# Kernel optimization log

Measured on AMD Instinct MI355X. Metric: run time of the kernel, lower is better.

## Reference

```python
import jax, jax.numpy as jnp
import numpy as np

H = 16          # num_heads
EPS = 1e-6      # RMSNorm eps


def setup_inputs() -> dict:
    key = jax.random.key(0)
    ks = jax.random.split(key, 5)
    B, N, D = 4, 4096, 1024
    x = jax.random.normal(ks[0], (B, N, D), dtype=jnp.float32)
    q = jax.random.normal(ks[1], (D,), dtype=jnp.float32)
    k = jax.random.normal(ks[2], (D,), dtype=jnp.float32)
    log_decay = jax.random.normal(ks[3], (H,), dtype=jnp.float32)
    norm_weight = jnp.ones((D,), dtype=jnp.float32)
    o_w = jax.random.normal(ks[4], (D, D), dtype=jnp.float32) * 0.02
    return {"x": x, "q": q, "k": k, "log_decay": log_decay,
            "norm_weight": norm_weight, "o_w": o_w}


def reference(x, q, k, log_decay, norm_weight, o_w):
    b, n, dm = x.shape
    dh = dm // H
    qh = q.reshape(H, dh)            # per-head query vector (constant over b, n)
    kh = k.reshape(H, dh)            # per-head key vector
    v = x.reshape(b, n, H, dh)       # values = input tokens
    # exp(logsigmoid(a)) == sigmoid(a): per-head decay in (0, 1)
    lam = jax.nn.sigmoid(log_decay)  # (H,)

    def step(S, v_t):
        # S: (b, H, dh, dh) recurrent state;  v_t: (b, H, dh)
        S = lam[None, :, None, None] * S + kh[None, :, :, None] * v_t[:, :, None, :]
        o_t = jnp.einsum('hd,bhdv->bhv', qh, S)
        return S, o_t

    S0 = jnp.zeros((b, H, dh, dh), dtype=x.dtype)
    _, o = jax.lax.scan(step, S0, jnp.moveaxis(v, 1, 0))  # o: (n, b, H, dh)
    o = jnp.moveaxis(o, 0, 1).reshape(b, n, dm)

    # RMSNorm over the channel dim
    o = o * jax.lax.rsqrt(jnp.mean(o * o, axis=-1, keepdims=True) + EPS) * norm_weight
    # o_proj (no bias)
    return o @ o_w.T
```

## Files before the change

### kernel.cpp

```cpp
#include <hip/hip_runtime.h>
#include <hip/hip_bf16.h>
#include <cstdint>
#include <cstddef>

#define HH   16
#define BB   4
#define NN   4096
#define DD   1024
#define MM   (BB * NN)
#define NC   128
#define LC   32
#define EPSV 1e-6f

typedef short short8 __attribute__((ext_vector_type(8)));
typedef float floatx4 __attribute__((ext_vector_type(4)));

__device__ __forceinline__ void async_copy16(const void* g, void* l) {
    __builtin_amdgcn_global_load_lds(
        (const __attribute__((address_space(1))) void*)g,
        (__attribute__((address_space(3))) void*)l, 16, 0, 0);
}

__device__ __forceinline__ uint2 pack_bf16x4(float a, float b, float c, float d) {
    union { __hip_bfloat16 h[4]; uint2 u; } cv;
    cv.h[0] = __float2bfloat16(a); cv.h[1] = __float2bfloat16(b);
    cv.h[2] = __float2bfloat16(c); cv.h[3] = __float2bfloat16(d);
    return cv.u;
}

__global__ void k_meta(const float* __restrict__ q, const float* __restrict__ k,
                       const float* __restrict__ ld, float* __restrict__ meta) {
    int tid = threadIdx.x;
    float p = q[tid] * k[tid];
    #pragma unroll
    for (int off = 32; off > 0; off >>= 1) p += __shfl_xor(p, off);
    if ((tid & 63) == 0) meta[16 + (tid >> 6)] = p;
    if (tid < HH) meta[tid] = 1.f / (1.f + expf(-ld[tid]));
}

__global__ void k_wconv(const float* __restrict__ ow, const float* __restrict__ nw,
                        __hip_bfloat16* __restrict__ wp) {
    size_t i4 = (size_t)blockIdx.x * 256 + threadIdx.x;
    int j = (int)((i4 * 4) & (DD - 1));
    float4 v = ((const float4*)ow)[i4];
    ((uint2*)wp)[i4] = pack_bf16x4(v.x * nw[j], v.y * nw[j + 1],
                                   v.z * nw[j + 2], v.w * nw[j + 3]);
}

__global__ void k_chunk_end(const float* __restrict__ x, const float* __restrict__ meta,
                            float* __restrict__ E) {
    int b = blockIdx.x >> 7, c = blockIdx.x & (NC - 1);
    int j4 = threadIdx.x;
    float lam = meta[(j4 * 4) >> 6];
    const float4* xp = (const float4*)(x + ((size_t)(b * NN + c * LC)) * DD) + j4;
    float4 e = {0.f, 0.f, 0.f, 0.f};
    #pragma unroll
    for (int t = 0; t < LC; ++t) {
        float4 v = xp[(size_t)t * (DD / 4)];
        e.x = fmaf(lam, e.x, v.x); e.y = fmaf(lam, e.y, v.y);
        e.z = fmaf(lam, e.z, v.z); e.w = fmaf(lam, e.w, v.w);
    }
    ((float4*)(E + (size_t)blockIdx.x * DD))[j4] = e;
}

__global__ void k_carry(const float* __restrict__ meta, const float* __restrict__ E,
                        float* __restrict__ P) {
    __shared__ float tile[NC][33];
    int b = blockIdx.x >> 5, jg = blockIdx.x & 31;
    int tid = threadIdx.x;
    int cc = tid >> 5, jj = tid & 31;
    #pragma unroll
    for (int it = 0; it < 16; ++it) {
        int c = it * 8 + cc;
        tile[c][jj] = E[(size_t)(b * NC + c) * DD + jg * 32 + jj];
    }
    __syncthreads();
    if (tid < 32) {
        int j = jg * 32 + tid;
        float lam = meta[j >> 6];
        float lamL = lam;
        lamL *= lamL; lamL *= lamL; lamL *= lamL; lamL *= lamL; lamL *= lamL;
        float p = 0.f;
        for (int c = 0; c < NC; ++c) {
            float e = tile[c][tid];
            tile[c][tid] = p;
            p = fmaf(lamL, p, e);
        }
    }
    __syncthreads();
    #pragma unroll
    for (int it = 0; it < 16; ++it) {
        int c = it * 8 + cc;
        P[(size_t)(b * NC + c) * DD + jg * 32 + jj] = tile[c][jj];
    }
}

__global__ void k_scan(const float* __restrict__ x, const float* __restrict__ meta,
                       const float* __restrict__ P, __hip_bfloat16* __restrict__ obf,
                       float* __restrict__ sumsq) {
    int b = blockIdx.x >> 7, c = blockIdx.x & (NC - 1);
    int j4 = threadIdx.x;
    int h = (j4 * 4) >> 6;
    float lam = meta[h];
    float ch  = meta[16 + h];
    int row0 = b * NN + c * LC;
    const float4* xp = (const float4*)(x + (size_t)row0 * DD) + j4;
    float4 y = ((const float4*)(P + (size_t)blockIdx.x * DD))[j4];
    int lane0 = ((threadIdx.x & 63) == 0);
    for (int t = 0; t < LC; ++t) {
        float4 v = xp[(size_t)t * (DD / 4)];
        y.x = fmaf(lam, y.x, v.x); y.y = fmaf(lam, y.y, v.y);
        y.z = fmaf(lam, y.z, v.z); y.w = fmaf(lam, y.w, v.w);
        float ox = ch * y.x, oy = ch * y.y, oz = ch * y.z, ow = ch * y.w;
        ((uint2*)(obf + (size_t)(row0 + t) * DD))[j4] = pack_bf16x4(ox, oy, oz, ow);
        float s = ox * ox + oy * oy + oz * oz + ow * ow;
        #pragma unroll
        for (int off = 32; off > 0; off >>= 1) s += __shfl_xor(s, off);
        if (lane0) atomicAdd(&sumsq[row0 + t], s);
    }
}

__launch_bounds__(256)
__global__ void k_gemm(const __hip_bfloat16* __restrict__ A,
                       const __hip_bfloat16* __restrict__ W,
                       const float* __restrict__ sumsq, float* __restrict__ out) {
    __shared__ __attribute__((aligned(16))) short sA[128 * 64];
    __shared__ __attribute__((aligned(16))) short sB[128 * 64];
    const int tid = threadIdx.x;
    const int l = tid & 63, w = tid >> 6;
    const int wm = w >> 1, wn = w & 1;
    const int g = blockIdx.x;
    const int bm = g & 127, bn = g >> 7;
    const int m0 = bm * 128, n0 = bn * 128;
    const short* Ag = (const short*)A;
    const short* Wg = (const short*)W;

    floatx4 acc[4][4] = {};

    int srow[4], scol[4];
    #pragma unroll
    for (int i = 0; i < 4; ++i) {
        int s = i * 256 + tid;
        srow[i] = s >> 3;
        scol[i] = ((s & 7) ^ ((s >> 3) & 7)) * 8;
    }

    for (int kt = 0; kt < 16; ++kt) {
        const int k0 = kt * 64;
        #pragma unroll
        for (int i = 0; i < 4; ++i) {
            async_copy16(Ag + (size_t)(m0 + srow[i]) * 1024 + k0 + scol[i],
                         (char*)sA + i * 4096 + w * 1024);
            async_copy16(Wg + (size_t)(n0 + srow[i]) * 1024 + k0 + scol[i],
                         (char*)sB + i * 4096 + w * 1024);
        }
        __syncthreads();
        #pragma unroll
        for (int ks = 0; ks < 2; ++ks) {
            short8 af[4], bf[4];
            #pragma unroll
            for (int mt = 0; mt < 4; ++mt) {
                int row = wm * 64 + mt * 16 + (l & 15);
                int c8  = (ks * 4 + (l >> 4)) ^ (row & 7);
                af[mt] = *(const short8*)(sA + row * 64 + c8 * 8);
            }
            #pragma unroll
            for (int nt = 0; nt < 4; ++nt) {
                int row = wn * 64 + nt * 16 + (l & 15);
                int c8  = (ks * 4 + (l >> 4)) ^ (row & 7);
                bf[nt] = *(const short8*)(sB + row * 64 + c8 * 8);
            }
            #pragma unroll
            for (int mt = 0; mt < 4; ++mt)
                #pragma unroll
                for (int nt = 0; nt < 4; ++nt)
                    acc[mt][nt] = __builtin_amdgcn_mfma_f32_16x16x32_bf16(af[mt], bf[nt], acc[mt][nt], 0, 0, 0);
        }
        __syncthreads();
    }

    #pragma unroll
    for (int mt = 0; mt < 4; ++mt) {
        #pragma unroll
        for (int r = 0; r < 4; ++r) {
            int mrow = m0 + wm * 64 + mt * 16 + (l >> 4) * 4 + r;
            float rs = rsqrtf(sumsq[mrow] * (1.f / 1024.f) + EPSV);
            #pragma unroll
            for (int nt = 0; nt < 4; ++nt) {
                int col = n0 + wn * 64 + nt * 16 + (l & 15);
                out[(size_t)mrow * 1024 + col] = acc[mt][nt][r] * rs;
            }
        }
    }
}

extern "C" void kernel_launch(void* const* d_in, const int* in_sizes, int n_in,
                              void* d_out, int out_size, void* d_ws, size_t ws_size,
                              hipStream_t stream) {
    const float* x  = (const float*)d_in[0];
    const float* q  = (const float*)d_in[1];
    const float* k  = (const float*)d_in[2];
    const float* ld = (const float*)d_in[3];
    const float* nw = (const float*)d_in[4];
    const float* ow = (const float*)d_in[5];
    float* out = (float*)d_out;

    char* ws = (char*)d_ws;
    float* meta  = (float*)(ws + 0);
    float* sumsq = (float*)(ws + 256);
    float* E     = (float*)(ws + 65792);
    float* P     = (float*)(ws + 2162944);
    __hip_bfloat16* Wp  = (__hip_bfloat16*)(ws + 4260096);
    __hip_bfloat16* Obf = (__hip_bfloat16*)(ws + 6357248);

    hipMemsetAsync(sumsq, 0, MM * sizeof(float), stream);
    k_meta<<<1, 1024, 0, stream>>>(q, k, ld, meta);
    k_wconv<<<(DD * DD / 4) / 256, 256, 0, stream>>>(ow, nw, Wp);
    k_chunk_end<<<BB * NC, 256, 0, stream>>>(x, meta, E);
    k_carry<<<BB * 32, 256, 0, stream>>>(meta, E, P);
    k_scan<<<BB * NC, 256, 0, stream>>>(x, meta, P, Obf, sumsq);
    k_gemm<<<(MM / 128) * (DD / 128), 256, 0, stream>>>(Obf, Wp, sumsq, out);
}
```

Before: 190.2 us.

## Double-buffer GEMM tiles, drop scan atomics, halve chunk length, fuse prep kernels

The GEMM now double-buffers its LDS tiles. The next K-tile is prefetched asynchronously while MFMAs run on the current one, which removes one barrier per iteration. The scan reduces per-row sum of squares through shared memory and writes it directly, so the atomics and the memset go away. Chunk length drops from 32 to 16 to give more parallel blocks. The carry pass now runs in place on E, and the meta and weight-conversion kernels are merged into one launch. The double buffer doubles GEMM LDS use, which may lower occupancy, and the smaller chunks make the serial carry scan longer.

New measurement: 193.0 us. Within noise of the previous version (+1.5%).

```diff
diff --git a/kernel.cpp b/kernel.cpp
--- a/kernel.cpp
+++ b/kernel.cpp
@@ -8,8 +8,8 @@
 #define NN   4096
 #define DD   1024
 #define MM   (BB * NN)
-#define NC   128
-#define LC   32
+#define NC   256
+#define LC   16
 #define EPSV 1e-6f
 
 typedef short short8 __attribute__((ext_vector_type(8)));
@@ -28,28 +28,31 @@
     return cv.u;
 }
 
-__global__ void k_meta(const float* __restrict__ q, const float* __restrict__ k,
-                       const float* __restrict__ ld, float* __restrict__ meta) {
+__global__ void k_prep(const float* __restrict__ ow, const float* __restrict__ nw,
+                       const float* __restrict__ q, const float* __restrict__ k,
+                       const float* __restrict__ ld,
+                       __hip_bfloat16* __restrict__ wp, float* __restrict__ meta) {
     int tid = threadIdx.x;
-    float p = q[tid] * k[tid];
-    #pragma unroll
-    for (int off = 32; off > 0; off >>= 1) p += __shfl_xor(p, off);
-    if ((tid & 63) == 0) meta[16 + (tid >> 6)] = p;
+    if (blockIdx.x < 1024) {
+        size_t i4 = (size_t)blockIdx.x * 256 + tid;
+        int j = (int)((i4 * 4) & (DD - 1));
+        float4 v = ((const float4*)ow)[i4];
+        ((uint2*)wp)[i4] = pack_bf16x4(v.x * nw[j], v.y * nw[j + 1],
+                                       v.z * nw[j + 2], v.w * nw[j + 3]);
+        return;
+    }
+    float p = 0.f;
+    #pragma unroll
+    for (int i = 0; i < 4; ++i) p += q[tid * 4 + i] * k[tid * 4 + i];
+    #pragma unroll
+    for (int off = 1; off < 16; off <<= 1) p += __shfl_xor(p, off);
+    if ((tid & 15) == 0) meta[16 + (tid >> 4)] = p;
     if (tid < HH) meta[tid] = 1.f / (1.f + expf(-ld[tid]));
-}
-
-__global__ void k_wconv(const float* __restrict__ ow, const float* __restrict__ nw,
-                        __hip_bfloat16* __restrict__ wp) {
-    size_t i4 = (size_t)blockIdx.x * 256 + threadIdx.x;
-    int j = (int)((i4 * 4) & (DD - 1));
-    float4 v = ((const float4*)ow)[i4];
-    ((uint2*)wp)[i4] = pack_bf16x4(v.x * nw[j], v.y * nw[j + 1],
-                                   v.z * nw[j + 2], v.w * nw[j + 3]);
 }
 
 __global__ void k_chunk_end(const float* __restrict__ x, const float* __restrict__ meta,
                             float* __restrict__ E) {
-    int b = blockIdx.x >> 7, c = blockIdx.x & (NC - 1);
+    int b = blockIdx.x >> 8, c = blockIdx.x & (NC - 1);
     int j4 = threadIdx.x;
     float lam = meta[(j4 * 4) >> 6];
     const float4* xp = (const float4*)(x + ((size_t)(b * NN + c * LC)) * DD) + j4;
@@ -63,14 +66,13 @@
     ((float4*)(E + (size_t)blockIdx.x * DD))[j4] = e;
 }
 
-__global__ void k_carry(const float* __restrict__ meta, const float* __restrict__ E,
-                        float* __restrict__ P) {
+__global__ void k_carry(const float* __restrict__ meta, float* __restrict__ E) {
     __shared__ float tile[NC][33];
     int b = blockIdx.x >> 5, jg = blockIdx.x & 31;
     int tid = threadIdx.x;
     int cc = tid >> 5, jj = tid & 31;
     #pragma unroll
-    for (int it = 0; it < 16; ++it) {
+    for (int it = 0; it < 32; ++it) {
         int c = it * 8 + cc;
         tile[c][jj] = E[(size_t)(b * NC + c) * DD + jg * 32 + jj];
     }
@@ -79,7 +81,7 @@
         int j = jg * 32 + tid;
         float lam = meta[j >> 6];
         float lamL = lam;
-        lamL *= lamL; lamL *= lamL; lamL *= lamL; lamL *= lamL; lamL *= lamL;
+        lamL *= lamL; lamL *= lamL; lamL *= lamL; lamL *= lamL;
         float p = 0.f;
         for (int c = 0; c < NC; ++c) {
             float e = tile[c][tid];
@@ -89,24 +91,26 @@
     }
     __syncthreads();
     #pragma unroll
-    for (int it = 0; it < 16; ++it) {
+    for (int it = 0; it < 32; ++it) {
         int c = it * 8 + cc;
-        P[(size_t)(b * NC + c) * DD + jg * 32 + jj] = tile[c][jj];
+        E[(size_t)(b * NC + c) * DD + jg * 32 + jj] = tile[c][jj];
     }
 }
 
 __global__ void k_scan(const float* __restrict__ x, const float* __restrict__ meta,
                        const float* __restrict__ P, __hip_bfloat16* __restrict__ obf,
                        float* __restrict__ sumsq) {
-    int b = blockIdx.x >> 7, c = blockIdx.x & (NC - 1);
+    __shared__ float wpart[LC][5];
+    int b = blockIdx.x >> 8, c = blockIdx.x & (NC - 1);
     int j4 = threadIdx.x;
+    int w = threadIdx.x >> 6;
     int h = (j4 * 4) >> 6;
     float lam = meta[h];
     float ch  = meta[16 + h];
     int row0 = b * NN + c * LC;
     const float4* xp = (const float4*)(x + (size_t)row0 * DD) + j4;
     float4 y = ((const float4*)(P + (size_t)blockIdx.x * DD))[j4];
-    int lane0 = ((threadIdx.x & 63) == 0);
+    #pragma unroll
     for (int t = 0; t < LC; ++t) {
         float4 v = xp[(size_t)t * (DD / 4)];
         y.x = fmaf(lam, y.x, v.x); y.y = fmaf(lam, y.y, v.y);
@@ -116,7 +120,12 @@
         float s = ox * ox + oy * oy + oz * oz + ow * ow;
         #pragma unroll
         for (int off = 32; off > 0; off >>= 1) s += __shfl_xor(s, off);
-        if (lane0) atomicAdd(&sumsq[row0 + t], s);
+        if ((threadIdx.x & 63) == 0) wpart[t][w] = s;
+    }
+    __syncthreads();
+    if (threadIdx.x < LC) {
+        int t = threadIdx.x;
+        sumsq[row0 + t] = wpart[t][0] + wpart[t][1] + wpart[t][2] + wpart[t][3];
     }
 }
 
@@ -124,8 +133,8 @@
 __global__ void k_gemm(const __hip_bfloat16* __restrict__ A,
                        const __hip_bfloat16* __restrict__ W,
                        const float* __restrict__ sumsq, float* __restrict__ out) {
-    __shared__ __attribute__((aligned(16))) short sA[128 * 64];
-    __shared__ __attribute__((aligned(16))) short sB[128 * 64];
+    __shared__ __attribute__((aligned(16))) short sA[2][128 * 64];
+    __shared__ __attribute__((aligned(16))) short sB[2][128 * 64];
     const int tid = threadIdx.x;
     const int l = tid & 63, w = tid >> 6;
     const int wm = w >> 1, wn = w & 1;
@@ -145,16 +154,27 @@
         scol[i] = ((s & 7) ^ ((s >> 3) & 7)) * 8;
     }
 
+    #pragma unroll
+    for (int i = 0; i < 4; ++i) {
+        async_copy16(Ag + (size_t)(m0 + srow[i]) * 1024 + scol[i],
+                     (char*)sA[0] + i * 4096 + w * 1024);
+        async_copy16(Wg + (size_t)(n0 + srow[i]) * 1024 + scol[i],
+                     (char*)sB[0] + i * 4096 + w * 1024);
+    }
+
     for (int kt = 0; kt < 16; ++kt) {
-        const int k0 = kt * 64;
-        #pragma unroll
-        for (int i = 0; i < 4; ++i) {
-            async_copy16(Ag + (size_t)(m0 + srow[i]) * 1024 + k0 + scol[i],
-                         (char*)sA + i * 4096 + w * 1024);
-            async_copy16(Wg + (size_t)(n0 + srow[i]) * 1024 + k0 + scol[i],
-                         (char*)sB + i * 4096 + w * 1024);
-        }
+        const int cur = kt & 1;
         __syncthreads();
+        if (kt < 15) {
+            const int nxt = cur ^ 1, k0 = (kt + 1) * 64;
+            #pragma unroll
+            for (int i = 0; i < 4; ++i) {
+                async_copy16(Ag + (size_t)(m0 + srow[i]) * 1024 + k0 + scol[i],
+                             (char*)sA[nxt] + i * 4096 + w * 1024);
+                async_copy16(Wg + (size_t)(n0 + srow[i]) * 1024 + k0 + scol[i],
+                             (char*)sB[nxt] + i * 4096 + w * 1024);
+            }
+        }
         #pragma unroll
         for (int ks = 0; ks < 2; ++ks) {
             short8 af[4], bf[4];
@@ -162,13 +182,13 @@
             for (int mt = 0; mt < 4; ++mt) {
                 int row = wm * 64 + mt * 16 + (l & 15);
                 int c8  = (ks * 4 + (l >> 4)) ^ (row & 7);
-                af[mt] = *(const short8*)(sA + row * 64 + c8 * 8);
+                af[mt] = *(const short8*)(&sA[cur][0] + row * 64 + c8 * 8);
             }
             #pragma unroll
             for (int nt = 0; nt < 4; ++nt) {
                 int row = wn * 64 + nt * 16 + (l & 15);
                 int c8  = (ks * 4 + (l >> 4)) ^ (row & 7);
-                bf[nt] = *(const short8*)(sB + row * 64 + c8 * 8);
+                bf[nt] = *(const short8*)(&sB[cur][0] + row * 64 + c8 * 8);
             }
             #pragma unroll
             for (int mt = 0; mt < 4; ++mt)
@@ -176,7 +196,6 @@
                 for (int nt = 0; nt < 4; ++nt)
                     acc[mt][nt] = __builtin_amdgcn_mfma_f32_16x16x32_bf16(af[mt], bf[nt], acc[mt][nt], 0, 0, 0);
         }
-        __syncthreads();
     }
 
     #pragma unroll
@@ -209,15 +228,12 @@
     float* meta  = (float*)(ws + 0);
     float* sumsq = (float*)(ws + 256);
     float* E     = (float*)(ws + 65792);
-    float* P     = (float*)(ws + 2162944);
     __hip_bfloat16* Wp  = (__hip_bfloat16*)(ws + 4260096);
     __hip_bfloat16* Obf = (__hip_bfloat16*)(ws + 6357248);
 
-    hipMemsetAsync(sumsq, 0, MM * sizeof(float), stream);
-    k_meta<<<1, 1024, 0, stream>>>(q, k, ld, meta);
-    k_wconv<<<(DD * DD / 4) / 256, 256, 0, stream>>>(ow, nw, Wp);
+    k_prep<<<1025, 256, 0, stream>>>(ow, nw, q, k, ld, Wp, meta);
     k_chunk_end<<<BB * NC, 256, 0, stream>>>(x, meta, E);
-    k_carry<<<BB * 32, 256, 0, stream>>>(meta, E, P);
-    k_scan<<<BB * NC, 256, 0, stream>>>(x, meta, P, Obf, sumsq);
+    k_carry<<<BB * 32, 256, 0, stream>>>(meta, E);
+    k_scan<<<BB * NC, 256, 0, stream>>>(x, meta, E, Obf, sumsq);
     k_gemm<<<(MM / 128) * (DD / 128), 256, 0, stream>>>(Obf, Wp, sumsq, out);
 }
```
